# Kernel optimization log

Measured on AMD Instinct MI355X. Metric: run time of the kernel, lower is better.

The kernel has to match this reference:

```python
import jax, jax.numpy as jnp
import numpy as np

HEADS = 8
DIM_HEAD = 64
SCALE = DIM_HEAD ** -0.5


def setup_inputs() -> dict:
    key = jax.random.key(0)
    ks = jax.random.split(key, 6)
    b, n, d = 2, 4096, 1024
    inner = HEADS * DIM_HEAD  # 512
    x = jax.random.normal(ks[0], (b, n, d), dtype=jnp.float32)
    Wq = jax.random.normal(ks[1], (d, inner), dtype=jnp.float32) * (d ** -0.5)
    Wk = jax.random.normal(ks[2], (d, inner), dtype=jnp.float32) * (d ** -0.5)
    Wv = jax.random.normal(ks[3], (d, inner), dtype=jnp.float32) * (d ** -0.5)
    Wout = jax.random.normal(ks[4], (inner, d), dtype=jnp.float32) * (inner ** -0.5)
    bout = jnp.zeros((d,), dtype=jnp.float32)
    return {"x": x, "Wq": Wq, "Wk": Wk, "Wv": Wv, "Wout": Wout, "bout": bout}


def reference(x, Wq, Wk, Wv, Wout, bout):
    b, n, _ = x.shape
    h, dh = HEADS, DIM_HEAD
    # self-attention: context = x
    q = (x @ Wq).reshape(b, n, h, dh).transpose(0, 2, 1, 3)  # b h n d
    k = (x @ Wk).reshape(b, n, h, dh).transpose(0, 2, 1, 3)
    v = (x @ Wv).reshape(b, n, h, dh).transpose(0, 2, 1, 3)
    sim = jnp.einsum('bhid,bhjd->bhij', q, k) * SCALE  # full score matrix
    attn = jax.nn.softmax(sim, axis=-1)
    out = jnp.einsum('bhij,bhjd->bhid', attn, v)
    out = out.transpose(0, 2, 1, 3).reshape(b, n, h * dh)  # b n (h d)
    return out @ Wout + bout
```

## Files before the change

kernel.cpp:

```cpp
#include <hip/hip_runtime.h>
#include <hip/hip_bf16.h>

typedef __bf16 bf16x8 __attribute__((ext_vector_type(8)));
typedef __bf16 bf16x4 __attribute__((ext_vector_type(4)));
typedef float floatx4 __attribute__((ext_vector_type(4)));

#define MFMA16(a, b, c) __builtin_amdgcn_mfma_f32_16x16x32_bf16((a), (b), (c), 0, 0, 0)

__device__ __forceinline__ void stage16(const __bf16* g, __bf16* lds_base) {
  __builtin_amdgcn_global_load_lds(
      (__attribute__((address_space(1))) void*)(void*)g,
      (__attribute__((address_space(3))) void*)lds_base, 16, 0, 0);
}

__global__ void detect_dtype(const unsigned int* __restrict__ x, int* __restrict__ flag) {
  __shared__ int cnt;
  if (threadIdx.x == 0) cnt = 0;
  __syncthreads();
  int c = 0;
  for (int i = threadIdx.x; i < 4096; i += 256) {
    const unsigned f = (x[i] >> 7) & 0xFF;
    c += (f >= 100 && f <= 140) ? 1 : 0;
  }
  atomicAdd(&cnt, c);
  __syncthreads();
  if (threadIdx.x == 0) *flag = (cnt > 2048) ? 1 : 0;
}

__global__ __launch_bounds__(256) void transpose3_conv(
    const void* __restrict__ s0, const void* __restrict__ s1,
    const void* __restrict__ s2, __bf16* __restrict__ dst,
    int R, int C, const int* __restrict__ flagp) {
  __shared__ __bf16 t[32][33];
  const int isbf = *flagp;
  const void* src = (blockIdx.z == 0) ? s0 : (blockIdx.z == 1) ? s1 : s2;
  __bf16* d = dst + (size_t)blockIdx.z * R * C;
  const int bx = blockIdx.x * 32, by = blockIdx.y * 32;
  const int x = threadIdx.x & 31, y0 = threadIdx.x >> 5;
#pragma unroll
  for (int i = y0; i < 32; i += 8) {
    const size_t idx = (size_t)(by + i) * C + bx + x;
    t[i][x] = isbf ? ((const __bf16*)src)[idx] : (__bf16)(((const float*)src)[idx]);
  }
  __syncthreads();
#pragma unroll
  for (int i = y0; i < 32; i += 8) d[(size_t)(bx + i) * R + by + x] = t[x][i];
}

__global__ __launch_bounds__(256) void transpose_conv(const void* __restrict__ src,
                                                      __bf16* __restrict__ dst,
                                                      int R, int C,
                                                      const int* __restrict__ flagp) {
  __shared__ __bf16 t[32][33];
  const int isbf = *flagp;
  const int bx = blockIdx.x * 32, by = blockIdx.y * 32;
  const int x = threadIdx.x & 31, y0 = threadIdx.x >> 5;
#pragma unroll
  for (int i = y0; i < 32; i += 8) {
    const size_t idx = (size_t)(by + i) * C + bx + x;
    t[i][x] = isbf ? ((const __bf16*)src)[idx] : (__bf16)(((const float*)src)[idx]);
  }
  __syncthreads();
#pragma unroll
  for (int i = y0; i < 32; i += 8) dst[(size_t)(bx + i) * R + by + x] = t[x][i];
}

__global__ __launch_bounds__(256) void vp_transpose(const __bf16* __restrict__ V,
                                                    __bf16* __restrict__ VP) {
  alignas(16) __shared__ __bf16 t[64][64];
  const int bh = blockIdx.y, s0 = blockIdx.x * 64;
  const int row = threadIdx.x >> 2, part = threadIdx.x & 3;
  const __bf16* src = V + (size_t)bh * 262144 + (size_t)(s0 + row) * 64 + part * 16;
  *(bf16x8*)&t[row][part * 16] = *(const bf16x8*)src;
  *(bf16x8*)&t[row][part * 16 + 8] = *(const bf16x8*)(src + 8);
  __syncthreads();
  const int d = row, og = part;
  bf16x8 w0, w1;
#pragma unroll
  for (int e = 0; e < 8; e++) {
    const int o0 = og * 16 + e, o1 = og * 16 + 8 + e;
    w0[e] = t[(o0 & 3) * 16 + (o0 >> 2)][d];
    w1[e] = t[(o1 & 3) * 16 + (o1 >> 2)][d];
  }
  __bf16* dst = VP + (size_t)bh * 262144 + (size_t)d * 4096 + s0 + og * 16;
  *(bf16x8*)dst = w0;
  *(bf16x8*)(dst + 8) = w1;
}

template <int A_DUAL>
__global__ __launch_bounds__(256) void gemm_bt(
    const void* __restrict__ Araw, const __bf16* __restrict__ Bt,
    void* __restrict__ Cv, void* __restrict__ Cv2, int M, int N, int K,
    const void* __restrict__ bias, int permute, int egress_dual,
    size_t zsB, size_t zsC, const int* __restrict__ flagp) {
  alignas(16) __shared__ __bf16 As[128 * 32];
  alignas(16) __shared__ __bf16 Bs[128 * 32];
  const int isbf = *flagp;
  Bt += blockIdx.z * zsB;
  const size_t zoff = (size_t)blockIdx.z * zsC;
  const int tid = threadIdx.x;
  const int wave = tid >> 6, lane = tid & 63;
  const int m0 = blockIdx.y * 128, n0 = blockIdx.x * 128;
  const int wm = (wave & 1) * 64, wn = (wave >> 1) * 64;
  const int fr = lane & 15, fq = lane >> 4;

  const floatx4 zero4 = {0.f, 0.f, 0.f, 0.f};
  floatx4 acc[4][4];
#pragma unroll
  for (int i = 0; i < 4; i++)
#pragma unroll
    for (int j = 0; j < 4; j++) acc[i][j] = zero4;

  const int lrow = lane >> 2;
  const int lk = (lane & 3) * 8;

  for (int k0 = 0; k0 < K; k0 += 32) {
#pragma unroll
    for (int cc = 0; cc < 2; ++cc) {
      const int c = 2 * wave + cc;
      const size_t aoff = (size_t)(m0 + c * 16 + lrow) * K + k0 + lk;
      if (A_DUAL && !isbf) {
        const float* p = (const float*)Araw + aoff;
        const float4 f0 = *(const float4*)p;
        const float4 f1 = *(const float4*)(p + 4);
        bf16x8 v;
        v[0] = (__bf16)f0.x; v[1] = (__bf16)f0.y; v[2] = (__bf16)f0.z; v[3] = (__bf16)f0.w;
        v[4] = (__bf16)f1.x; v[5] = (__bf16)f1.y; v[6] = (__bf16)f1.z; v[7] = (__bf16)f1.w;
        *(bf16x8*)&As[c * 512 + lane * 8] = v;
      } else {
        stage16((const __bf16*)Araw + aoff, &As[c * 512]);
      }
      stage16(Bt + (size_t)(n0 + c * 16 + lrow) * K + k0 + lk, &Bs[c * 512]);
    }
    __syncthreads();
    bf16x8 af[4], bg[4];
#pragma unroll
    for (int mt = 0; mt < 4; mt++)
      af[mt] = *(const bf16x8*)&As[(wm + mt * 16 + fr) * 32 + fq * 8];
#pragma unroll
    for (int nt = 0; nt < 4; nt++)
      bg[nt] = *(const bf16x8*)&Bs[(wn + nt * 16 + fr) * 32 + fq * 8];
#pragma unroll
    for (int mt = 0; mt < 4; mt++)
#pragma unroll
      for (int nt = 0; nt < 4; nt++)
        acc[mt][nt] = MFMA16(af[mt], bg[nt], acc[mt][nt]);
    __syncthreads();
  }

  const float qs = (permute && blockIdx.z == 0) ? 0.18033688011112042f
                                                : 1.0f;
#pragma unroll
  for (int mt = 0; mt < 4; mt++)
#pragma unroll
    for (int nt = 0; nt < 4; nt++)
#pragma unroll
      for (int r = 0; r < 4; r++) {
        const int row = m0 + wm + mt * 16 + fq * 4 + r;
        const int col = n0 + wn + nt * 16 + fr;
        float v = acc[mt][nt][r] * qs;
        if (bias)
          v += isbf ? (float)((const __bf16*)bias)[col] : ((const float*)bias)[col];
        if (permute) {
          const int bh = (row >> 12) * 8 + (col >> 6);
          const int s = row & 4095, d = col & 63;
          const size_t pidx = (size_t)bh * 262144 + (size_t)s * 64 + d;
          if (blockIdx.z == 2)
            ((__bf16*)Cv2)[pidx] = (__bf16)v;
          else
            ((__bf16*)Cv)[zoff + pidx] = (__bf16)v;
        } else {
          const size_t idx = (size_t)row * N + col;
          if (egress_dual && !isbf)
            ((float*)Cv)[idx] = v;
          else
            ((__bf16*)Cv)[idx] = (__bf16)v;
        }
      }
}

#define ATT_S 4096
__global__ __launch_bounds__(256) void attn_flash(
    const __bf16* __restrict__ Qa, const __bf16* __restrict__ Ka,
    const __bf16* __restrict__ VPa, __bf16* __restrict__ Oa) {
  alignas(16) __shared__ __bf16 Kl[2][64 * 64];
  alignas(16) __shared__ __bf16 Vl[2][64 * 64];
  alignas(16) __shared__ __bf16 Pl[4 * 32 * 64];
  const int tid = threadIdx.x, wave = tid >> 6, lane = tid & 63;
  const int bh = blockIdx.y, b = bh >> 3, h = bh & 7;
  const int q0 = blockIdx.x * 128 + wave * 32;
  const int fr = lane & 15, fq = lane >> 4;
  const __bf16* Qb = Qa + (size_t)bh * ATT_S * 64;
  const __bf16* Kb = Ka + (size_t)bh * ATT_S * 64;
  const __bf16* Vb = VPa + (size_t)bh * ATT_S * 64;

  const int sw0 = ((fq ^ (fr & 7)) * 8);
  const int sw1 = (((fq + 4) ^ (fr & 7)) * 8);
  const int r0 = tid >> 3;
  const int ssw = (((tid & 7) ^ (r0 & 7)) * 8);

  __bf16* const Pw_base = &Pl[0];

  bf16x8 aq[2][2];
#pragma unroll
  for (int mt = 0; mt < 2; mt++)
#pragma unroll
    for (int kt = 0; kt < 2; kt++)
      aq[mt][kt] = *(const bf16x8*)(Qb + (size_t)(q0 + mt * 16 + fr) * 64 + kt * 32 + fq * 8);

  const floatx4 zero4 = {0.f, 0.f, 0.f, 0.f};
  floatx4 o[2][4];
  float lsum[2][4];
#pragma unroll
  for (int mt = 0; mt < 2; mt++) {
#pragma unroll
    for (int nt = 0; nt < 4; nt++) o[mt][nt] = zero4;
#pragma unroll
    for (int r = 0; r < 4; r++) lsum[mt][r] = 0.f;
  }

#pragma unroll
  for (int c = 0; c < 2; c++) {
    stage16(Kb + (size_t)(c * 32 + r0) * 64 + ssw, &Kl[0][(c * 256 + wave * 64) * 8]);
    stage16(Vb + (size_t)(c * 32 + r0) * 4096 + 0 + ssw, &Vl[0][(c * 256 + wave * 64) * 8]);
  }

  for (int j = 0; j < ATT_S / 64; ++j) {
    __syncthreads();
    const int cur = j & 1;
    if (j + 1 < ATT_S / 64) {
      const int kv1 = (j + 1) * 64;
#pragma unroll
      for (int c = 0; c < 2; c++) {
        stage16(Kb + (size_t)(kv1 + c * 32 + r0) * 64 + ssw,
                &Kl[1 - cur][(c * 256 + wave * 64) * 8]);
        stage16(Vb + (size_t)(c * 32 + r0) * 4096 + kv1 + ssw,
                &Vl[1 - cur][(c * 256 + wave * 64) * 8]);
      }
    }
    const __bf16* Klc = Kl[cur];
    const __bf16* Vlc = Vl[cur];

    floatx4 s4[2][4];
#pragma unroll
    for (int nt = 0; nt < 4; nt++) {
      bf16x8 bk0 = *(const bf16x8*)&Klc[(nt * 16 + fr) * 64 + sw0];
      bf16x8 bk1 = *(const bf16x8*)&Klc[(nt * 16 + fr) * 64 + sw1];
#pragma unroll
      for (int mt = 0; mt < 2; mt++) {
        floatx4 z = zero4;
        z = MFMA16(aq[mt][0], bk0, z);
        z = MFMA16(aq[mt][1], bk1, z);
        s4[mt][nt] = z;
      }
    }

#pragma unroll
    for (int mt = 0; mt < 2; mt++)
#pragma unroll
      for (int r = 0; r < 4; r++) {
        bf16x4 pv;
        float psum = 0.f;
#pragma unroll
        for (int nt = 0; nt < 4; nt++) {
          const float p = __builtin_amdgcn_exp2f(s4[mt][nt][r]);
          pv[nt] = (__bf16)p;
          psum += p;
        }
        lsum[mt][r] += psum;
        const int row = wave * 32 + mt * 16 + fq * 4 + r;
        const int vg = (fr >> 1) ^ ((fq * 4 + r) & 7);
        *(bf16x4*)&Pw_base[row * 64 + vg * 8 + (fr & 1) * 4] = pv;
      }
    asm volatile("s_waitcnt lgkmcnt(0)" ::: "memory");

    bf16x8 bv[4][2];
#pragma unroll
    for (int nt = 0; nt < 4; nt++) {
      bv[nt][0] = *(const bf16x8*)&Vlc[(nt * 16 + fr) * 64 + sw0];
      bv[nt][1] = *(const bf16x8*)&Vlc[(nt * 16 + fr) * 64 + sw1];
    }
#pragma unroll
    for (int mt = 0; mt < 2; mt++) {
      const int prow = (wave * 32 + mt * 16 + fr) * 64;
      bf16x8 ap0 = *(const bf16x8*)&Pl[prow + sw0];
      bf16x8 ap1 = *(const bf16x8*)&Pl[prow + sw1];
#pragma unroll
      for (int nt = 0; nt < 4; nt++) {
        o[mt][nt] = MFMA16(ap0, bv[nt][0], o[mt][nt]);
        o[mt][nt] = MFMA16(ap1, bv[nt][1], o[mt][nt]);
      }
    }
  }

#pragma unroll
  for (int off = 1; off < 16; off <<= 1)
#pragma unroll
    for (int mt = 0; mt < 2; mt++)
#pragma unroll
      for (int r = 0; r < 4; r++) lsum[mt][r] += __shfl_xor(lsum[mt][r], off, 64);

#pragma unroll
  for (int mt = 0; mt < 2; mt++)
#pragma unroll
    for (int nt = 0; nt < 4; nt++)
#pragma unroll
      for (int r = 0; r < 4; r++) {
        const int row = q0 + mt * 16 + fq * 4 + r;
        const int col = h * 64 + nt * 16 + fr;
        const float v = o[mt][nt][r] / lsum[mt][r];
        Oa[(size_t)(b * ATT_S + row) * 512 + col] = (__bf16)v;
      }
}

extern "C" void kernel_launch(void* const* d_in, const int* in_sizes, int n_in,
                              void* d_out, int out_size, void* d_ws, size_t ws_size,
                              hipStream_t stream) {
  (void)in_sizes; (void)n_in; (void)out_size; (void)ws_size;
  const void* x = d_in[0];
  const void* Wq = d_in[1];
  const void* Wk = d_in[2];
  const void* Wv = d_in[3];
  const void* Wout = d_in[4];
  const void* bout = d_in[5];

  char* ws = (char*)d_ws;
  int* flag = (int*)ws;
  __bf16* wtq = (__bf16*)(ws + (1u << 20));
  __bf16* wto = (__bf16*)(ws + (4u << 20));
  __bf16* Q = (__bf16*)(ws + (5u << 20));
  __bf16* K = (__bf16*)(ws + (13u << 20));
  __bf16* VP = (__bf16*)(ws + (21u << 20));
  __bf16* O = (__bf16*)(ws + (29u << 20));
  __bf16* Vtmp = O;

  detect_dtype<<<1, 256, 0, stream>>>((const unsigned int*)x, flag);

  transpose3_conv<<<dim3(16, 32, 3), 256, 0, stream>>>(Wq, Wk, Wv, wtq, 1024, 512, flag);
  transpose_conv<<<dim3(32, 16), 256, 0, stream>>>(Wout, wto, 512, 1024, flag);

  gemm_bt<1><<<dim3(4, 64, 3), 256, 0, stream>>>(
      x, wtq, Q, Vtmp, 8192, 512, 1024, nullptr, 1, 0,
      (size_t)512 * 1024, (size_t)8192 * 512, flag);

  vp_transpose<<<dim3(64, 16), 256, 0, stream>>>(Vtmp, VP);

  attn_flash<<<dim3(32, 16), 256, 0, stream>>>(Q, K, VP, O);

  gemm_bt<0><<<dim3(8, 64, 1), 256, 0, stream>>>(
      O, wto, d_out, nullptr, 8192, 1024, 512, bout, 0, 1, 0, 0, flag);
}
```

Measured before the change: 293.5 us.

## Split attention KV range across two blocks and add combine kernel

The flash attention kernel now splits the key/value sequence into two halves via a grid z dimension. Each half writes unnormalized fp32 partial outputs and row sums to workspace. A new combine kernel adds the halves, normalizes and writes bf16 output. This doubles the attention block count to fill more CUs, at the cost of extra fp32 global traffic and one more kernel launch.

```diff
diff --git a/kernel.cpp b/kernel.cpp
--- a/kernel.cpp
+++ b/kernel.cpp
@@ -180,14 +180,17 @@
 }
 
 #define ATT_S 4096
+#define KV_SPLIT 2
 __global__ __launch_bounds__(256) void attn_flash(
     const __bf16* __restrict__ Qa, const __bf16* __restrict__ Ka,
-    const __bf16* __restrict__ VPa, __bf16* __restrict__ Oa) {
+    const __bf16* __restrict__ VPa, float* __restrict__ Of,
+    float* __restrict__ lp) {
   alignas(16) __shared__ __bf16 Kl[2][64 * 64];
   alignas(16) __shared__ __bf16 Vl[2][64 * 64];
   alignas(16) __shared__ __bf16 Pl[4 * 32 * 64];
   const int tid = threadIdx.x, wave = tid >> 6, lane = tid & 63;
   const int bh = blockIdx.y, b = bh >> 3, h = bh & 7;
+  const int z = blockIdx.z;
   const int q0 = blockIdx.x * 128 + wave * 32;
   const int fr = lane & 15, fq = lane >> 4;
   const __bf16* Qb = Qa + (size_t)bh * ATT_S * 64;
@@ -199,8 +202,6 @@
   const int r0 = tid >> 3;
   const int ssw = (((tid & 7) ^ (r0 & 7)) * 8);
 
-  __bf16* const Pw_base = &Pl[0];
-
   bf16x8 aq[2][2];
 #pragma unroll
   for (int mt = 0; mt < 2; mt++)
@@ -219,17 +220,22 @@
     for (int r = 0; r < 4; r++) lsum[mt][r] = 0.f;
   }
 
+  const int JT = (ATT_S / 64) / KV_SPLIT;
+  const int jbase = z * JT;
+
 #pragma unroll
   for (int c = 0; c < 2; c++) {
-    stage16(Kb + (size_t)(c * 32 + r0) * 64 + ssw, &Kl[0][(c * 256 + wave * 64) * 8]);
-    stage16(Vb + (size_t)(c * 32 + r0) * 4096 + 0 + ssw, &Vl[0][(c * 256 + wave * 64) * 8]);
-  }
-
-  for (int j = 0; j < ATT_S / 64; ++j) {
+    stage16(Kb + (size_t)(jbase * 64 + c * 32 + r0) * 64 + ssw,
+            &Kl[0][(c * 256 + wave * 64) * 8]);
+    stage16(Vb + (size_t)(c * 32 + r0) * 4096 + jbase * 64 + ssw,
+            &Vl[0][(c * 256 + wave * 64) * 8]);
+  }
+
+  for (int j = 0; j < JT; ++j) {
     __syncthreads();
     const int cur = j & 1;
-    if (j + 1 < ATT_S / 64) {
-      const int kv1 = (j + 1) * 64;
+    if (j + 1 < JT) {
+      const int kv1 = (jbase + j + 1) * 64;
 #pragma unroll
       for (int c = 0; c < 2; c++) {
         stage16(Kb + (size_t)(kv1 + c * 32 + r0) * 64 + ssw,
@@ -248,10 +254,10 @@
       bf16x8 bk1 = *(const bf16x8*)&Klc[(nt * 16 + fr) * 64 + sw1];
 #pragma unroll
       for (int mt = 0; mt < 2; mt++) {
-        floatx4 z = zero4;
-        z = MFMA16(aq[mt][0], bk0, z);
-        z = MFMA16(aq[mt][1], bk1, z);
-        s4[mt][nt] = z;
+        floatx4 zz = zero4;
+        zz = MFMA16(aq[mt][0], bk0, zz);
+        zz = MFMA16(aq[mt][1], bk1, zz);
+        s4[mt][nt] = zz;
       }
     }
 
@@ -270,7 +276,7 @@
         lsum[mt][r] += psum;
         const int row = wave * 32 + mt * 16 + fq * 4 + r;
         const int vg = (fr >> 1) ^ ((fq * 4 + r) & 7);
-        *(bf16x4*)&Pw_base[row * 64 + vg * 8 + (fr & 1) * 4] = pv;
+        *(bf16x4*)&Pl[row * 64 + vg * 8 + (fr & 1) * 4] = pv;
       }
     asm volatile("s_waitcnt lgkmcnt(0)" ::: "memory");
 
@@ -300,17 +306,40 @@
 #pragma unroll
       for (int r = 0; r < 4; r++) lsum[mt][r] += __shfl_xor(lsum[mt][r], off, 64);
 
+  float* Ofz = Of + (size_t)z * 8192 * 512;
+  float* lz = lp + (size_t)z * 16 * 4096;
 #pragma unroll
   for (int mt = 0; mt < 2; mt++)
 #pragma unroll
-    for (int nt = 0; nt < 4; nt++)
-#pragma unroll
-      for (int r = 0; r < 4; r++) {
-        const int row = q0 + mt * 16 + fq * 4 + r;
+    for (int r = 0; r < 4; r++) {
+      const int row = q0 + mt * 16 + fq * 4 + r;
+      if (fr == 0) lz[bh * 4096 + row] = lsum[mt][r];
+#pragma unroll
+      for (int nt = 0; nt < 4; nt++) {
         const int col = h * 64 + nt * 16 + fr;
-        const float v = o[mt][nt][r] / lsum[mt][r];
-        Oa[(size_t)(b * ATT_S + row) * 512 + col] = (__bf16)v;
-      }
+        Ofz[(size_t)(b * ATT_S + row) * 512 + col] = o[mt][nt][r];
+      }
+    }
+}
+
+__global__ __launch_bounds__(256) void attn_combine(
+    const float* __restrict__ Of, const float* __restrict__ lp,
+    __bf16* __restrict__ O) {
+  const size_t i = ((size_t)blockIdx.x * 256 + threadIdx.x) * 8;
+  const int row = (int)(i >> 9), colb = (int)(i & 511);
+  const int bh = (row >> 12) * 8 + (colb >> 6), qrow = row & 4095;
+  const float l = lp[bh * 4096 + qrow] + lp[16 * 4096 + bh * 4096 + qrow];
+  const float inv = 1.0f / l;
+  const float4 a0 = *(const float4*)(Of + i);
+  const float4 a1 = *(const float4*)(Of + i + 4);
+  const float4 b0 = *(const float4*)(Of + 8192 * 512 + i);
+  const float4 b1 = *(const float4*)(Of + 8192 * 512 + i + 4);
+  bf16x8 w;
+  w[0] = (__bf16)((a0.x + b0.x) * inv); w[1] = (__bf16)((a0.y + b0.y) * inv);
+  w[2] = (__bf16)((a0.z + b0.z) * inv); w[3] = (__bf16)((a0.w + b0.w) * inv);
+  w[4] = (__bf16)((a1.x + b1.x) * inv); w[5] = (__bf16)((a1.y + b1.y) * inv);
+  w[6] = (__bf16)((a1.z + b1.z) * inv); w[7] = (__bf16)((a1.w + b1.w) * inv);
+  *(bf16x8*)(O + i) = w;
 }
 
 extern "C" void kernel_launch(void* const* d_in, const int* in_sizes, int n_in,
@@ -333,6 +362,8 @@
   __bf16* VP = (__bf16*)(ws + (21u << 20));
   __bf16* O = (__bf16*)(ws + (29u << 20));
   __bf16* Vtmp = O;
+  float* Of = (float*)(ws + (38u << 20));
+  float* lp = (float*)(ws + (72u << 20));
 
   detect_dtype<<<1, 256, 0, stream>>>((const unsigned int*)x, flag);
 
@@ -345,7 +376,9 @@
 
   vp_transpose<<<dim3(64, 16), 256, 0, stream>>>(Vtmp, VP);
 
-  attn_flash<<<dim3(32, 16), 256, 0, stream>>>(Q, K, VP, O);
+  attn_flash<<<dim3(32, 16, KV_SPLIT), 256, 0, stream>>>(Q, K, VP, Of, lp);
+
+  attn_combine<<<2048, 256, 0, stream>>>(Of, lp, O);
 
   gemm_bt<0><<<dim3(8, 64, 1), 256, 0, stream>>>(
       O, wto, d_out, nullptr, 8192, 1024, 512, bout, 0, 1, 0, 0, flag);
```

Result: no change. 291.3 us (-0.7%).
